# Optimization experiments

Hardware: AMD Instinct MI355X
Metric: run time of the kernel (lower is better)

The kernel has to match this reference:

```python
import jax, jax.numpy as jnp
import numpy as np

GRID = 64
ECC = 10.0
ATT_CTR = (3.0, 0.0)
NORM_SIGMA = 0.5


def _grids():
    coords = jnp.linspace(-ECC, ECC, GRID, dtype=jnp.float32)
    X, Y = jnp.meshgrid(coords, coords)          # (64,64)
    RF_X = X.reshape(-1)                         # (4096,) one RF center per grid point
    RF_Y = Y.reshape(-1)
    return X, Y, RF_X, RF_Y


def _fields(X, Y, RF_X, RF_Y, sigma):
    # Batched Gaussian fields: (64,64,4096), each normalized to unit sum.
    d2 = (X[:, :, None] - RF_X) ** 2 + (Y[:, :, None] - RF_Y) ** 2
    g = jnp.exp(-d2 / (2.0 * sigma ** 2))
    return g / jnp.sum(g, axis=(0, 1), keepdims=True)


def setup_inputs() -> dict:
    key = jax.random.key(0)
    ks = jax.random.split(key, 2)
    stim = jax.random.uniform(ks[0], (GRID, GRID, 256), dtype=jnp.float32)
    return {
        "stim": stim,
        "prf_sigma_scale_factor": jnp.float32(0.2),
        "attention_field_sigma": jnp.float32(2.0),
        "attention_field_gain": jnp.float32(4.0),
        "suppressive_surround_sigma_factor": jnp.float32(3.0),
        "summation_field_sigma_factor": jnp.float32(2.0),
    }


def reference(stim, prf_sigma_scale_factor, attention_field_sigma,
              attention_field_gain, suppressive_surround_sigma_factor,
              summation_field_sigma_factor):
    X, Y, RF_X, RF_Y = _grids()
    if stim.ndim != 3:
        stim = stim[:, :, None]

    # Attention field: unnormalized Gaussian, flattened, gain*g + 1.
    att = jnp.exp(-((X - ATT_CTR[0]) ** 2 + (Y - ATT_CTR[1]) ** 2)
                  / (2.0 * attention_field_sigma ** 2)).reshape(-1)  # (4096,)
    attfield = attention_field_gain * att + 1.0

    rf_sigma = 0.07 + prf_sigma_scale_factor * jnp.sqrt(RF_X ** 2 + RF_Y ** 2)  # (4096,)

    receptive_field = _fields(X, Y, RF_X, RF_Y, rf_sigma)                                  # (64,64,4096)
    suppressive_surround = _fields(X, Y, RF_X, RF_Y, rf_sigma * suppressive_surround_sigma_factor).reshape(GRID * GRID, -1)
    summation_field = _fields(X, Y, RF_X, RF_Y, rf_sigma * summation_field_sigma_factor).reshape(GRID * GRID, -1)

    stimulus_drive = jnp.einsum('ijk,ija->ka', receptive_field, stim)   # (4096, a)
    numerator = stimulus_drive * attfield[:, None]                      # (4096, a)
    surroundresponse = suppressive_surround.T @ numerator               # (4096, a)
    predicted_neural = numerator / (surroundresponse + NORM_SIGMA)
    predicted_voxel = summation_field.T @ predicted_neural
    # voxel_lookup_indices is identity (voxeldata=None), so lookups are no-ops.
    return (numerator, surroundresponse, predicted_neural, predicted_voxel)
```

## Files before the change

kernel.cpp:

```cpp
#include <hip/hip_runtime.h>
#include <hip/hip_bf16.h>
#include <math.h>

#define NP 4096
#define NA 256

typedef unsigned short ushort_t;
typedef __attribute__((ext_vector_type(8))) short short8;
typedef __attribute__((ext_vector_type(4))) float f32x4;
typedef __attribute__((ext_vector_type(8))) unsigned short ushort8v;

__device__ __forceinline__ ushort_t f2bf(float x) {
    __hip_bfloat16 h = __float2bfloat16(x);
    return *reinterpret_cast<ushort_t*>(&h);
}
__device__ __forceinline__ float bf2f(ushort_t u) {
    unsigned x = ((unsigned)u) << 16;
    return __builtin_bit_cast(float, x);
}

__global__ __launch_bounds__(512)
void setup_all(const float* __restrict__ stim,
               const float* __restrict__ pscale,
               const float* __restrict__ pasig,
               const float* __restrict__ pagain,
               const float* __restrict__ pssf,
               const float* __restrict__ psff,
               ushort_t* __restrict__ stimT,
               ushort_t* __restrict__ gxbI,
               float* __restrict__ gy2I,
               float* __restrict__ attI)
{
    __shared__ float lt[64 * 68];
    const int t = threadIdx.x;
    const int bx = blockIdx.x;
    const float step = 20.0f / 63.0f;

    if (bx < 256) {
        const int g0 = (bx & 63) * 64, a0 = (bx >> 6) * 64;
        const int gr = t >> 3, ar = (t & 7) * 8;
        *(f32x4*)&lt[gr * 68 + ar]     = *(const f32x4*)&stim[(size_t)(g0 + gr) * NA + a0 + ar];
        *(f32x4*)&lt[gr * 68 + ar + 4] = *(const f32x4*)&stim[(size_t)(g0 + gr) * NA + a0 + ar + 4];
        __syncthreads();
        const int a = t >> 3, c8 = (t & 7) * 8;
        ushort8v u;
        #pragma unroll
        for (int i = 0; i < 8; ++i) u[i] = f2bf(lt[(c8 + i) * 68 + a]);
        *(ushort8v*)&stimT[(size_t)(a0 + a) * NP + g0 + c8] = u;
    } else {
        const int b    = bx - 256;
        const int f    = b >> 6;
        const int pblk = b & 63;
        const int w    = t >> 6;
        const int l    = t & 63;
        const float sc_scale = pscale[0];
        const float fac = (f == 0) ? 1.0f : (f == 1 ? pssf[0] : psff[0]);
        const float coord = -10.0f + step * (float)l;
        ushort_t* gxb = gxbI + ((size_t)f * 64 + pblk) * 4096;
        float*    gy2 = gy2I + ((size_t)f * 64 + pblk) * 4096;

        #pragma unroll
        for (int i = 0; i < 8; ++i) {
            const int pl = w * 8 + i, p = pblk * 64 + pl;
            float cx = -10.0f + step * (float)(p & 63);
            float cy = -10.0f + step * (float)(p >> 6);
            float sg = (0.07f + sc_scale * sqrtf(cx * cx + cy * cy)) * fac;
            float inv = 1.0f / (2.0f * sg * sg);
            float dx = coord - cx, dy = coord - cy;
            float ex = expf(-dx * dx * inv);
            float ey = expf(-dy * dy * inv);
            float sx = ex, sy = ey;
            #pragma unroll
            for (int o = 32; o > 0; o >>= 1) {
                sx += __shfl_xor(sx, o);
                sy += __shfl_xor(sy, o);
            }
            gxb[pl * 64 + l] = f2bf(ex / sx);
            gy2[l * 64 + (((pl & 15) * 4) ^ ((l & 7) << 3)) + (pl >> 4)] = ey / sy;
            if (f == 0 && l == 0) {
                float asig = pasig[0];
                float d2 = (cx - 3.0f) * (cx - 3.0f) + cy * cy;
                attI[p] = pagain[0] * expf(-d2 / (2.0f * asig * asig)) + 1.0f;
            }
        }
    }
}

template <int MODE>
__global__ __launch_bounds__(512)
void field_gemm(const ushort_t* __restrict__ bT,
                const ushort_t* __restrict__ gxbF,
                const float* __restrict__ gy2F,
                const float* __restrict__ attI,
                const float* __restrict__ num,
                float* __restrict__ C,
                float* __restrict__ C2,
                ushort_t* __restrict__ CT,
                const ushort_t* __restrict__ numTsrc)
{
    __shared__ __align__(16) unsigned char smem[147712];
    ushort_t* lB   = (ushort_t*)smem;
    float*    lgy2 = (float*)(smem + 131072);
    float*    latt = (float*)(smem + 147456);

    const int t    = threadIdx.x;
    const int w    = t >> 6;
    const int l    = t & 63;
    const int asub = w >> 1;
    const int kh   = w & 1;
    const int r16  = l & 15;
    const int q    = l >> 4;
    const int srow  = l >> 3;
    const int sslot = (l & 7) ^ (srow & 7);

    const int v    = blockIdx.x;
    const int lid  = (v & 7) * 32 + (v >> 3);
    const int pblk = lid & 63;
    const int p0   = pblk * 64;
    const int a0   = (lid >> 6) * 64;

#define STAGE(buf, tt)                                                         \
    _Pragma("unroll")                                                          \
    for (int h = 0; h < 2; ++h) {                                              \
        const ushort_t* src = bT + (size_t)(a0 + w * 8 + srow) * NP            \
                              + (2 * (tt) + h) * 64 + sslot * 8;               \
        ushort_t* dst = lB + ((buf) * 2 + h) * 4096 + (w * 8) * 64;            \
        __builtin_amdgcn_global_load_lds(                                      \
            (const __attribute__((address_space(1))) unsigned int*)src,        \
            (__attribute__((address_space(3))) unsigned int*)dst, 16, 0, 0);   \
    }

    STAGE(0, 0); STAGE(1, 1); STAGE(2, 2); STAGE(3, 3);

    {
        const float* gsrc = gy2F + (size_t)pblk * 4096;
        #pragma unroll
        for (int r = 0; r < 2; ++r) {
            const float* src = gsrc + (w * 2 + r) * 256 + l * 4;
            float* dst = lgy2 + (w * 2 + r) * 256;
            __builtin_amdgcn_global_load_lds(
                (const __attribute__((address_space(1))) unsigned int*)src,
                (__attribute__((address_space(3))) unsigned int*)dst, 16, 0, 0);
        }
    }
    if (MODE == 0 && w == 0) {
        const float* src = attI + p0 + l;
        __builtin_amdgcn_global_load_lds(
            (const __attribute__((address_space(1))) unsigned int*)src,
            (__attribute__((address_space(3))) unsigned int*)latt, 4, 0, 0);
    }

    const ushort_t* gxb = gxbF + (size_t)pblk * 4096;
    short8 gxf[4][2];
    #pragma unroll
    for (int pt = 0; pt < 4; ++pt) {
        const int row = pt * 16 + r16;
        gxf[pt][0] = *(const short8*)&gxb[row * 64 + q * 8];
        gxf[pt][1] = *(const short8*)&gxb[row * 64 + 32 + q * 8];
    }

    __syncthreads();

    const int n   = asub * 16 + r16;
    const int bo0 = n * 64 + ((q ^ (n & 7)) * 8);
    const int bo1 = n * 64 + (((4 + q) ^ (n & 7)) * 8);

    f32x4 acc[4];
    #pragma unroll
    for (int pt = 0; pt < 4; ++pt) acc[pt] = (f32x4){0.f, 0.f, 0.f, 0.f};

    for (int ph = 0; ph < 16; ++ph) {
        if (ph <= 13) {
            STAGE((2 * ph + 4) & 7, 2 * ph + 4);
            STAGE((2 * ph + 5) & 7, 2 * ph + 5);
            asm volatile("s_waitcnt vmcnt(8)" ::: "memory");
        } else if (ph == 14) {
            asm volatile("s_waitcnt vmcnt(4)" ::: "memory");
        } else {
            asm volatile("s_waitcnt vmcnt(0)" ::: "memory");
        }
        __builtin_amdgcn_s_barrier();

        #pragma unroll
        for (int u = 0; u < 2; ++u) {
            const int tt = 2 * ph + u;
            const ushort_t* bb = lB + ((tt & 7) * 2 + kh) * 4096;
            short8 A0 = *(const short8*)(bb + bo0);
            short8 A1 = *(const short8*)(bb + bo1);
            const int gi = 2 * tt + kh;
            f32x4 s4 = *(const f32x4*)(lgy2 + gi * 64 +
                                       ((r16 * 4) ^ ((gi & 7) << 3)));
            __builtin_amdgcn_s_setprio(1);
            #pragma unroll
            for (int pt = 0; pt < 4; ++pt) {
                f32x4 tmp = (f32x4){0.f, 0.f, 0.f, 0.f};
                tmp = __builtin_amdgcn_mfma_f32_16x16x32_bf16(A0, gxf[pt][0], tmp, 0, 0, 0);
                tmp = __builtin_amdgcn_mfma_f32_16x16x32_bf16(A1, gxf[pt][1], tmp, 0, 0, 0);
                float sc = s4[pt];
                acc[pt] += tmp * sc;
            }
            __builtin_amdgcn_s_setprio(0);
        }
    }
#undef STAGE

    __syncthreads();
    float* lred_ap = (float*)smem;
    float* lred_pa = (float*)(smem + 34816);

    const int a_base = asub * 16 + q * 4;
    #pragma unroll
    for (int pt = 0; pt < 4; ++pt) {
        const int p_idx = pt * 16 + r16;
        *(f32x4*)&lred_pa[(kh * 64 + p_idx) * 68 + a_base] = acc[pt];
        #pragma unroll
        for (int r = 0; r < 4; ++r)
            lred_ap[(kh * 64 + a_base + r) * 68 + p_idx] = acc[pt][r];
    }
    __syncthreads();

    if (MODE != 2) {
        const int aL = t >> 3, p8 = (t & 7) * 8;
        f32x4 s0 = *(f32x4*)&lred_ap[aL * 68 + p8] +
                   *(f32x4*)&lred_ap[(64 + aL) * 68 + p8];
        f32x4 s1 = *(f32x4*)&lred_ap[aL * 68 + p8 + 4] +
                   *(f32x4*)&lred_ap[(64 + aL) * 68 + p8 + 4];
        ushort8v cv;
        if (MODE == 0) {
            f32x4 t0 = *(f32x4*)&latt[p8];
            f32x4 t1 = *(f32x4*)&latt[p8 + 4];
            s0 *= t0; s1 *= t1;
            #pragma unroll
            for (int r = 0; r < 4; ++r) {
                cv[r] = f2bf(s0[r]);
                cv[4 + r] = f2bf(s1[r]);
            }
        } else {
            ushort8v nt = *(const ushort8v*)&numTsrc[(size_t)(a0 + aL) * NP + p0 + p8];
            #pragma unroll
            for (int r = 0; r < 4; ++r) {
                cv[r] = f2bf(bf2f(nt[r]) / (s0[r] + 0.5f));
                cv[4 + r] = f2bf(bf2f(nt[4 + r]) / (s1[r] + 0.5f));
            }
        }
        *(ushort8v*)&CT[(size_t)(a0 + aL) * NP + p0 + p8] = cv;
    }

    {
        const int pL = t >> 3, a8 = (t & 7) * 8;
        f32x4 s0 = *(f32x4*)&lred_pa[pL * 68 + a8] +
                   *(f32x4*)&lred_pa[(64 + pL) * 68 + a8];
        f32x4 s1 = *(f32x4*)&lred_pa[pL * 68 + a8 + 4] +
                   *(f32x4*)&lred_pa[(64 + pL) * 68 + a8 + 4];
        float* cbase = C + (size_t)(p0 + pL) * NA + a0 + a8;
        if (MODE == 0) {
            float att = latt[pL];
            s0 *= att; s1 *= att;
            *(f32x4*)cbase = s0;
            *(f32x4*)(cbase + 4) = s1;
        } else if (MODE == 1) {
            *(f32x4*)cbase = s0;
            *(f32x4*)(cbase + 4) = s1;
            const float* nb = num + (size_t)(p0 + pL) * NA + a0 + a8;
            f32x4 n0 = *(const f32x4*)nb;
            f32x4 n1 = *(const f32x4*)(nb + 4);
            f32x4 o0 = n0 / (s0 + 0.5f);
            f32x4 o1 = n1 / (s1 + 0.5f);
            float* c2 = C2 + (size_t)(p0 + pL) * NA + a0 + a8;
            *(f32x4*)c2 = o0;
            *(f32x4*)(c2 + 4) = o1;
        } else {
            *(f32x4*)cbase = s0;
            *(f32x4*)(cbase + 4) = s1;
        }
    }
}

extern "C" void kernel_launch(void* const* d_in, const int* in_sizes, int n_in,
                              void* d_out, int out_size, void* d_ws, size_t ws_size,
                              hipStream_t stream)
{
    const float* stim   = (const float*)d_in[0];
    const float* pscale = (const float*)d_in[1];
    const float* pasig  = (const float*)d_in[2];
    const float* pagain = (const float*)d_in[3];
    const float* pssf   = (const float*)d_in[4];
    const float* psff   = (const float*)d_in[5];

    float* out  = (float*)d_out;
    float* num  = out;
    float* surr = out + (size_t)NP * NA;
    float* pn   = out + 2 * (size_t)NP * NA;
    float* pv   = out + 3 * (size_t)NP * NA;

    ushort_t* stimT = (ushort_t*)d_ws;
    ushort_t* numT  = stimT + (size_t)NA * NP;
    ushort_t* pnT   = numT + (size_t)NA * NP;
    ushort_t* gxbI  = pnT + (size_t)NA * NP;
    float*    gy2I  = (float*)(gxbI + (size_t)3 * 64 * 4096);
    float*    attI  = gy2I + (size_t)3 * 64 * 4096;

    setup_all<<<448, 512, 0, stream>>>(stim, pscale, pasig, pagain, pssf, psff,
                                       stimT, gxbI, gy2I, attI);

    const ushort_t* gx0 = gxbI;
    const ushort_t* gx1 = gxbI + (size_t)64 * 4096;
    const ushort_t* gx2 = gxbI + (size_t)128 * 4096;
    const float*    gy0 = gy2I;
    const float*    gy1 = gy2I + (size_t)64 * 4096;
    const float*    gy2 = gy2I + (size_t)128 * 4096;

    field_gemm<0><<<256, 512, 0, stream>>>(stimT, gx0, gy0, attI, nullptr,
                                           num, nullptr, numT, nullptr);
    field_gemm<1><<<256, 512, 0, stream>>>(numT, gx1, gy1, attI, num,
                                           surr, pn, pnT, numT);
    field_gemm<2><<<256, 512, 0, stream>>>(pnT, gx2, gy2, attI, nullptr,
                                           pv, nullptr, nullptr, nullptr);
}
```

Before: 65.52 us.

## Make B-tile staging wave-private to drop per-step block barriers

Each wave now loads only the slice of the B tile it will read itself. Because of that, the main K loop no longer needs block-wide s_barrier calls and relies only on per-wave vmcnt waits. The prefetch distance grows from 4 to 6 tiles within the 8-buffer ring, and the loop is restructured into per-tile steps that issue the next stage right after the MFMAs. This is meant to remove barrier stalls and skew between waves. The cost is more outstanding loads per wave and hand-tuned vmcnt counts that must exactly match the issued loads.

Result: faster. 58.99 us (-10.0%).

```diff
diff --git a/kernel.cpp b/kernel.cpp
--- a/kernel.cpp
+++ b/kernel.cpp
@@ -112,6 +112,7 @@
     const int q    = l >> 4;
     const int srow  = l >> 3;
     const int sslot = (l & 7) ^ (srow & 7);
+    const int base_w = kh * 4096 + asub * 1024;
 
     const int v    = blockIdx.x;
     const int lid  = (v & 7) * 32 + (v >> 3);
@@ -119,18 +120,19 @@
     const int p0   = pblk * 64;
     const int a0   = (lid >> 6) * 64;
 
-#define STAGE(buf, tt)                                                         \
+#define STAGE(buf, tn)                                                         \
     _Pragma("unroll")                                                          \
     for (int h = 0; h < 2; ++h) {                                              \
-        const ushort_t* src = bT + (size_t)(a0 + w * 8 + srow) * NP            \
-                              + (2 * (tt) + h) * 64 + sslot * 8;               \
-        ushort_t* dst = lB + ((buf) * 2 + h) * 4096 + (w * 8) * 64;            \
+        const ushort_t* src = bT + (size_t)(a0 + asub * 16 + h * 8 + srow) * NP\
+                              + (2 * (tn) + kh) * 64 + sslot * 8;              \
+        ushort_t* dst = lB + (buf) * 8192 + base_w + h * 512;                  \
         __builtin_amdgcn_global_load_lds(                                      \
             (const __attribute__((address_space(1))) unsigned int*)src,        \
             (__attribute__((address_space(3))) unsigned int*)dst, 16, 0, 0);   \
     }
 
-    STAGE(0, 0); STAGE(1, 1); STAGE(2, 2); STAGE(3, 3);
+    STAGE(0, 0); STAGE(1, 1); STAGE(2, 2);
+    STAGE(3, 3); STAGE(4, 4); STAGE(5, 5);
 
     {
         const float* gsrc = gy2F + (size_t)pblk * 4096;
@@ -161,47 +163,39 @@
 
     __syncthreads();
 
-    const int n   = asub * 16 + r16;
-    const int bo0 = n * 64 + ((q ^ (n & 7)) * 8);
-    const int bo1 = n * 64 + (((4 + q) ^ (n & 7)) * 8);
+    const int bo0 = r16 * 64 + ((q ^ (r16 & 7)) * 8);
+    const int bo1 = r16 * 64 + (((4 + q) ^ (r16 & 7)) * 8);
 
     f32x4 acc[4];
     #pragma unroll
     for (int pt = 0; pt < 4; ++pt) acc[pt] = (f32x4){0.f, 0.f, 0.f, 0.f};
 
-    for (int ph = 0; ph < 16; ++ph) {
-        if (ph <= 13) {
-            STAGE((2 * ph + 4) & 7, 2 * ph + 4);
-            STAGE((2 * ph + 5) & 7, 2 * ph + 5);
-            asm volatile("s_waitcnt vmcnt(8)" ::: "memory");
-        } else if (ph == 14) {
-            asm volatile("s_waitcnt vmcnt(4)" ::: "memory");
-        } else {
-            asm volatile("s_waitcnt vmcnt(0)" ::: "memory");
-        }
-        __builtin_amdgcn_s_barrier();
-
-        #pragma unroll
-        for (int u = 0; u < 2; ++u) {
-            const int tt = 2 * ph + u;
-            const ushort_t* bb = lB + ((tt & 7) * 2 + kh) * 4096;
-            short8 A0 = *(const short8*)(bb + bo0);
-            short8 A1 = *(const short8*)(bb + bo1);
-            const int gi = 2 * tt + kh;
-            f32x4 s4 = *(const f32x4*)(lgy2 + gi * 64 +
-                                       ((r16 * 4) ^ ((gi & 7) << 3)));
-            __builtin_amdgcn_s_setprio(1);
-            #pragma unroll
-            for (int pt = 0; pt < 4; ++pt) {
-                f32x4 tmp = (f32x4){0.f, 0.f, 0.f, 0.f};
-                tmp = __builtin_amdgcn_mfma_f32_16x16x32_bf16(A0, gxf[pt][0], tmp, 0, 0, 0);
-                tmp = __builtin_amdgcn_mfma_f32_16x16x32_bf16(A1, gxf[pt][1], tmp, 0, 0, 0);
-                float sc = s4[pt];
-                acc[pt] += tmp * sc;
-            }
-            __builtin_amdgcn_s_setprio(0);
-        }
-    }
+#define KSTEP(tt_, VM)                                                         \
+    {                                                                          \
+        const int tt_k = (tt_);                                                \
+        asm volatile("s_waitcnt vmcnt(" #VM ")" ::: "memory");                 \
+        const ushort_t* bb = lB + (tt_k & 7) * 8192 + base_w;                  \
+        short8 A0 = *(const short8*)(bb + bo0);                                \
+        short8 A1 = *(const short8*)(bb + bo1);                                \
+        const int gi = 2 * tt_k + kh;                                          \
+        f32x4 s4 = *(const f32x4*)(lgy2 + gi * 64 +                            \
+                                   ((r16 * 4) ^ ((gi & 7) << 3)));             \
+        __builtin_amdgcn_s_setprio(1);                                         \
+        _Pragma("unroll")                                                      \
+        for (int pt = 0; pt < 4; ++pt) {                                       \
+            f32x4 tmp = (f32x4){0.f, 0.f, 0.f, 0.f};                           \
+            tmp = __builtin_amdgcn_mfma_f32_16x16x32_bf16(A0, gxf[pt][0], tmp, 0, 0, 0); \
+            tmp = __builtin_amdgcn_mfma_f32_16x16x32_bf16(A1, gxf[pt][1], tmp, 0, 0, 0); \
+            float sc = s4[pt];                                                 \
+            acc[pt] += tmp * sc;                                               \
+        }                                                                      \
+        __builtin_amdgcn_s_setprio(0);                                         \
+        if (tt_k <= 25) { STAGE((tt_k + 6) & 7, tt_k + 6); }                   \
+    }
+
+    for (int tt = 0; tt < 27; ++tt) KSTEP(tt, 10);
+    KSTEP(27, 8); KSTEP(28, 6); KSTEP(29, 4); KSTEP(30, 2); KSTEP(31, 0);
+#undef KSTEP
 #undef STAGE
 
     __syncthreads();
```
